# Optimization experiments

Hardware: AMD Instinct MI355X
Metric: run time of the kernel (lower is better)

## Reference

```python
import jax, jax.numpy as jnp
import numpy as np

H = 10                 # heads in both convs
EPS = 1e-5             # GraphNorm eps
N, E, D_NODE, D_EDGE, G = 100000, 1600000, 128, 32, 64


def _lin(key, out_d, in_d, bias=True):
    k1, k2 = jax.random.split(key)
    W = jax.random.normal(k1, (out_d, in_d), jnp.float32) / np.sqrt(in_d)
    if bias:
        b = jax.random.normal(k2, (out_d,), jnp.float32) * 0.01
        return W, b
    return W


def setup_inputs() -> dict:
    key = jax.random.key(0)
    ks = jax.random.split(key, 20)
    x = jax.random.normal(ks[0], (N, D_NODE), jnp.float32)
    edge_attr = jax.random.normal(ks[1], (E, D_EDGE), jnp.float32)
    edge_index = jax.random.randint(ks[2], (2, E), 0, N)
    batch_idx = jnp.sort(jax.random.randint(ks[3], (N,), 0, G))
    # conv1: in=128, out=5, heads=10
    q1W, q1b = _lin(ks[4], H * 5, D_NODE)
    k1W, k1b = _lin(ks[5], H * 5, D_NODE)
    v1W, v1b = _lin(ks[6], H * 5, D_NODE)
    e1W = _lin(ks[7], H * 5, D_EDGE, bias=False)
    s1W, s1b = _lin(ks[8], 5, D_NODE)        # lin_skip
    b1W = _lin(ks[9], 1, 3 * 5, bias=False)  # lin_beta
    # GraphNorm(5)
    gnW = jnp.ones((5,), jnp.float32)
    gnb = jnp.zeros((5,), jnp.float32)
    gnms = jnp.ones((5,), jnp.float32)       # mean_scale
    # conv2: in=5, out=1, heads=10
    q2W, q2b = _lin(ks[10], H * 1, 5)
    k2W, k2b = _lin(ks[11], H * 1, 5)
    v2W, v2b = _lin(ks[12], H * 1, 5)
    e2W = _lin(ks[13], H * 1, D_EDGE, bias=False)
    s2W, s2b = _lin(ks[14], 1, 5)
    b2W = _lin(ks[15], 1, 3 * 1, bias=False)
    return dict(x=x, edge_attr=edge_attr, edge_index=edge_index, batch_idx=batch_idx,
                q1W=q1W, q1b=q1b, k1W=k1W, k1b=k1b, v1W=v1W, v1b=v1b, e1W=e1W,
                s1W=s1W, s1b=s1b, b1W=b1W, gnW=gnW, gnb=gnb, gnms=gnms,
                q2W=q2W, q2b=q2b, k2W=k2W, k2b=k2b, v2W=v2W, v2b=v2b, e2W=e2W,
                s2W=s2W, s2b=s2b, b2W=b2W)


def _tconv(x, src, dst, edge_attr, qW, qb, kW, kb, vW, vb, eW, sW, sb, bW, c):
    """PyG TransformerConv: concat=False, beta=True, eval (dropout off)."""
    n = x.shape[0]
    q = (x @ qW.T + qb).reshape(n, H, c)
    k = (x @ kW.T + kb).reshape(n, H, c)
    v = (x @ vW.T + vb).reshape(n, H, c)
    e = (edge_attr @ eW.T).reshape(-1, H, c)            # [E,H,c]
    kj = k[src] + e                                      # gather + edge bias
    alpha = jnp.einsum('ehc,ehc->eh', q[dst], kj) / np.sqrt(c)
    amax = jax.lax.stop_gradient(jax.ops.segment_max(alpha, dst, num_segments=n))
    ex = jnp.exp(alpha - amax[dst])
    denom = jax.ops.segment_sum(ex, dst, num_segments=n)
    a = ex / denom[dst]                                  # segment softmax [E,H]
    out = jax.ops.segment_sum((v[src] + e) * a[:, :, None], dst, num_segments=n)
    out = out.mean(axis=1)                               # concat=False -> head mean [N,c]
    xr = x @ sW.T + sb                                   # skip
    beta = jax.nn.sigmoid(jnp.concatenate([out, xr, out - xr], -1) @ bW.T)
    return beta * xr + (1.0 - beta) * out


def _graph_norm(x, batch, w, b, ms):
    cnt = jnp.maximum(jax.ops.segment_sum(jnp.ones((x.shape[0],), x.dtype), batch,
                                          num_segments=G), 1.0)[:, None]
    mean = jax.ops.segment_sum(x, batch, num_segments=G) / cnt
    out = x - mean[batch] * ms
    var = jax.ops.segment_sum(out * out, batch, num_segments=G) / cnt
    return w * out / jnp.sqrt(var + EPS)[batch] + b


def reference(x, edge_attr, edge_index, batch_idx,
              q1W, q1b, k1W, k1b, v1W, v1b, e1W, s1W, s1b, b1W,
              gnW, gnb, gnms,
              q2W, q2b, k2W, k2b, v2W, v2b, e2W, s2W, s2b, b2W):
    src, dst = edge_index[0], edge_index[1]
    h = _tconv(x, src, dst, edge_attr, q1W, q1b, k1W, k1b, v1W, v1b, e1W,
               s1W, s1b, b1W, 5)
    h = jax.nn.relu(_graph_norm(h, batch_idx, gnW, gnb, gnms))
    out = _tconv(h, src, dst, edge_attr, q2W, q2b, k2W, k2b, v2W, v2b, e2W,
                 s2W, s2b, b2W, 1)
    return jax.nn.sigmoid(out)
```

## Files before the change

### kernel.cpp

```cpp
#include <hip/hip_runtime.h>
#include <math.h>


#define EPS 1e-5f
#define INV_SQRT5 0.44721359549995794f

__device__ __forceinline__ float f16_to_f32(unsigned short u) {
  union { unsigned short us; _Float16 h; } cv; cv.us = u;
  return (float)cv.h;
}

__device__ __forceinline__ void store40(const float (&acc)[40], int n, int g,
                                        float* __restrict__ q1, float* __restrict__ kv1,
                                        float* __restrict__ xr1) {
#pragma unroll
  for (int c = 0; c < 40; ++c) {
    int ch = g * 40 + c;
    if (ch < 50)        q1[(size_t)n * 52 + ch] = acc[c];
    else if (ch < 100)  kv1[(size_t)n * 104 + 2 * (ch - 50)] = acc[c];
    else if (ch < 150)  kv1[(size_t)n * 104 + 2 * (ch - 100) + 1] = acc[c];
    else if (ch < 155)  xr1[(size_t)n * 8 + (ch - 150)] = acc[c];
  }
}

__global__ __launch_bounds__(256, 4) void k_qkvs1(
    const float* __restrict__ x,
    const float* __restrict__ qW, const float* __restrict__ qb,
    const float* __restrict__ kW, const float* __restrict__ kb,
    const float* __restrict__ vW, const float* __restrict__ vb,
    const float* __restrict__ sW, const float* __restrict__ sb,
    float* __restrict__ q1, float* __restrict__ kv1,
    float* __restrict__ xr1, int n_nodes) {
  __shared__ __align__(16) float sWt[40 * 128];
  __shared__ float sB[40];
  const int t = threadIdx.x;
  const int g = blockIdx.y;
  const int n0 = blockIdx.x * 512;

  for (int i = t; i < 1280; i += 256) {
    int c = i >> 5, q = i & 31;
    int ch = g * 40 + c;
    float4 w = make_float4(0.f, 0.f, 0.f, 0.f);
    const float* srcr = nullptr;
    if (ch < 50)        srcr = qW + ch * 128;
    else if (ch < 100)  srcr = kW + (ch - 50) * 128;
    else if (ch < 150)  srcr = vW + (ch - 100) * 128;
    else if (ch < 155)  srcr = sW + (ch - 150) * 128;
    if (srcr) w = *(const float4*)(srcr + q * 4);
    *(float4*)&sWt[c * 128 + q * 4] = w;
  }
  if (t < 40) {
    int ch = g * 40 + t;
    float b = 0.f;
    if (ch < 50) b = qb[ch];
    else if (ch < 100) b = kb[ch - 50];
    else if (ch < 150) b = vb[ch - 100];
    else if (ch < 155) b = sb[ch - 150];
    sB[t] = b;
  }
  __syncthreads();

  float accA[40], accB[40];
#pragma unroll
  for (int c = 0; c < 40; ++c) { accA[c] = sB[c]; accB[c] = sB[c]; }
  const int na = n0 + 2 * t, nb = na + 1;
  const bool okA = na < n_nodes, okB = nb < n_nodes;
  const float* xa_p = x + (size_t)(okA ? na : 0) * 128;
  const float* xb_p = x + (size_t)(okB ? nb : 0) * 128;
  const float4* w4 = (const float4*)sWt;

  for (int kc = 0; kc < 128; kc += 8) {
    float4 xa0 = *(const float4*)(xa_p + kc);
    float4 xa1 = *(const float4*)(xa_p + kc + 4);
    float4 xb0 = *(const float4*)(xb_p + kc);
    float4 xb1 = *(const float4*)(xb_p + kc + 4);
    const int base = kc >> 2;
#pragma unroll
    for (int c = 0; c < 40; ++c) {
      float4 w0 = w4[c * 32 + base];
      float4 w1 = w4[c * 32 + base + 1];
      accA[c] = fmaf(w0.x, xa0.x, accA[c]); accA[c] = fmaf(w0.y, xa0.y, accA[c]);
      accA[c] = fmaf(w0.z, xa0.z, accA[c]); accA[c] = fmaf(w0.w, xa0.w, accA[c]);
      accA[c] = fmaf(w1.x, xa1.x, accA[c]); accA[c] = fmaf(w1.y, xa1.y, accA[c]);
      accA[c] = fmaf(w1.z, xa1.z, accA[c]); accA[c] = fmaf(w1.w, xa1.w, accA[c]);
      accB[c] = fmaf(w0.x, xb0.x, accB[c]); accB[c] = fmaf(w0.y, xb0.y, accB[c]);
      accB[c] = fmaf(w0.z, xb0.z, accB[c]); accB[c] = fmaf(w0.w, xb0.w, accB[c]);
      accB[c] = fmaf(w1.x, xb1.x, accB[c]); accB[c] = fmaf(w1.y, xb1.y, accB[c]);
      accB[c] = fmaf(w1.w, xb1.w, accB[c]); accB[c] = fmaf(w1.z, xb1.z, accB[c]);
    }
  }
  if (okA) store40(accA, na, g, q1, kv1, xr1);
  if (okB) store40(accB, nb, g, q1, kv1, xr1);
}

__global__ __launch_bounds__(256) void k_hist(const int* __restrict__ ei, int n_edges,
                                              int* __restrict__ cnt) {
  int e = blockIdx.x * 256 + threadIdx.x;
  if (e < n_edges) atomicAdd(&cnt[ei[n_edges + e]], 1);
}

__global__ __launch_bounds__(256) void k_scansum(const int* __restrict__ cnt,
                                                 int* __restrict__ bsum, int n) {
  int base = blockIdx.x * 1024 + threadIdx.x * 4;
  int s = 0;
  if (base + 3 < n) {
    int4 v = *(const int4*)(cnt + base);
    s = v.x + v.y + v.z + v.w;
  } else {
    for (int i = base; i < n && i < base + 4; ++i) s += cnt[i];
  }
#pragma unroll
  for (int off = 32; off; off >>= 1) s += __shfl_down(s, off);
  __shared__ int wsum[4];
  if ((threadIdx.x & 63) == 0) wsum[threadIdx.x >> 6] = s;
  __syncthreads();
  if (threadIdx.x == 0) bsum[blockIdx.x] = wsum[0] + wsum[1] + wsum[2] + wsum[3];
}

__global__ __launch_bounds__(256) void k_scantop(int* __restrict__ bsum, int nb) {
  __shared__ int ls[256];
  int tid = threadIdx.x;
  int v = (tid < nb) ? bsum[tid] : 0;
  ls[tid] = v;
  __syncthreads();
  for (int off = 1; off < 256; off <<= 1) {
    int t = (tid >= off) ? ls[tid - off] : 0;
    __syncthreads();
    ls[tid] += t;
    __syncthreads();
  }
  if (tid < nb) bsum[tid] = ls[tid] - v;
}

__global__ __launch_bounds__(256) void k_scanout(const int* __restrict__ cnt,
                                                 const int* __restrict__ bsum,
                                                 int* __restrict__ rp,
                                                 int* __restrict__ cursor, int n) {
  const int tid = threadIdx.x;
  const int lane = tid & 63;
  const int w = tid >> 6;
  int base = blockIdx.x * 1024 + tid * 4;
  int c0 = 0, c1 = 0, c2 = 0, c3 = 0;
  if (base + 3 < n) {
    int4 v = *(const int4*)(cnt + base);
    c0 = v.x; c1 = v.y; c2 = v.z; c3 = v.w;
  } else if (base < n) {
    c0 = cnt[base];
    if (base + 1 < n) c1 = cnt[base + 1];
    if (base + 2 < n) c2 = cnt[base + 2];
    if (base + 3 < n) c3 = cnt[base + 3];
  }
  int s = c0 + c1 + c2 + c3;
  int incl = s;
#pragma unroll
  for (int off = 1; off < 64; off <<= 1) {
    int t = __shfl_up(incl, off);
    if (lane >= off) incl += t;
  }
  __shared__ int wsum[4];
  if (lane == 63) wsum[w] = incl;
  __syncthreads();
  int woff = 0;
#pragma unroll
  for (int j = 0; j < 3; ++j) if (j < w) woff += wsum[j];
  int excl = bsum[blockIdx.x] + woff + (incl - s);
  int4 o;
  o.x = excl; o.y = o.x + c0; o.z = o.y + c1; o.w = o.z + c2;
  if (base + 3 < n) {
    *(int4*)(rp + base) = o;
    *(int4*)(cursor + base) = o;
  } else if (base < n) {
    rp[base] = o.x; cursor[base] = o.x;
    if (base + 1 < n) { rp[base + 1] = o.y; cursor[base + 1] = o.y; }
    if (base + 2 < n) { rp[base + 2] = o.z; cursor[base + 2] = o.z; }
  }
  if (base < n && base + 4 >= n) rp[n] = excl + s;
}

__global__ __launch_bounds__(256) void k_scatter(const int* __restrict__ ei, int n_edges,
                                                 int* __restrict__ cursor,
                                                 int* __restrict__ seid,
                                                 int* __restrict__ ssrc) {
  int e = blockIdx.x * 256 + threadIdx.x;
  if (e >= n_edges) return;
  int s = ei[e];
  int d = ei[n_edges + e];
  int p = atomicAdd(&cursor[d], 1);
  seid[p] = e;
  ssrc[p] = s;
}

__global__ __launch_bounds__(256) void k_evt(
    float* attr, const float* __restrict__ e1W, const float* __restrict__ e2W,
    int n_edges) {
  int e = blockIdx.x * 256 + threadIdx.x;
  if (e >= n_edges) return;
  const float4* ar = (const float4*)(attr + (size_t)e * 32);
  float4 a[8];
#pragma unroll
  for (int j = 0; j < 8; ++j) a[j] = ar[j];
  unsigned int d[30];
#pragma unroll
  for (int c2 = 0; c2 < 30; ++c2) {
    int c0 = 2 * c2, c1 = 2 * c2 + 1;
    const float* w0 = (c0 < 50) ? (e1W + c0 * 32) : (e2W + (c0 - 50) * 32);
    const float* w1 = (c1 < 50) ? (e1W + c1 * 32) : (e2W + (c1 - 50) * 32);
    float acc0 = 0.f, acc1 = 0.f;
#pragma unroll
    for (int j = 0; j < 8; ++j) {
      float4 wa = *(const float4*)(w0 + 4 * j);
      float4 wb = *(const float4*)(w1 + 4 * j);
      acc0 = fmaf(wa.x, a[j].x, acc0); acc0 = fmaf(wa.y, a[j].y, acc0);
      acc0 = fmaf(wa.z, a[j].z, acc0); acc0 = fmaf(wa.w, a[j].w, acc0);
      acc1 = fmaf(wb.x, a[j].x, acc1); acc1 = fmaf(wb.y, a[j].y, acc1);
      acc1 = fmaf(wb.z, a[j].z, acc1); acc1 = fmaf(wb.w, a[j].w, acc1);
    }
    union { _Float16 h[2]; unsigned int u; } p;
    p.h[0] = (_Float16)acc0; p.h[1] = (_Float16)acc1;
    d[c2] = p.u;
  }
  unsigned int* row = (unsigned int*)(attr + (size_t)e * 32);
#pragma unroll
  for (int k = 0; k < 7; ++k)
    *(uint4*)(row + 4 * k) = make_uint4(d[4 * k], d[4 * k + 1], d[4 * k + 2], d[4 * k + 3]);
  *(uint2*)(row + 28) = make_uint2(d[28], d[29]);
}

__global__ __launch_bounds__(256) void k_conv1(
    const int* __restrict__ rp, const int* __restrict__ seid,
    const int* __restrict__ ssrc, const float* __restrict__ attr,
    const float* __restrict__ q1, const float* __restrict__ kv1,
    const float* __restrict__ xr1,
    const float* __restrict__ bW, float* __restrict__ h1, int n_nodes) {
  const int lane = threadIdx.x & 63;
  const int wid = (blockIdx.x * 256 + threadIdx.x) >> 6;
  const int nw = gridDim.x * 4;
  const int wr = (lane < 50) ? lane : 0;
  const int g0 = (wr / 5) * 5;
  const int cp = lane % 5;
  const unsigned short* evr = (const unsigned short*)attr;

  for (int n = wid; n < n_nodes; n += nw) {
    const int p0 = rp[n], deg = rp[n + 1] - p0;
    const float qc = q1[(size_t)n * 52 + wr];
    int eL = 0, sL = 0;
    if (lane < deg) { eL = seid[p0 + lane]; sL = ssrc[p0 + lane]; }
    float accN0 = 0.f, accD0 = 0.f, accN1 = 0.f, accD1 = 0.f;
    int i = 0;
    for (; i + 2 <= deg; i += 2) {
      int e0, s0, e1, s1;
      if (i + 1 < 64) {
        e0 = __shfl(eL, i);     s0 = __shfl(sL, i);
        e1 = __shfl(eL, i + 1); s1 = __shfl(sL, i + 1);
      } else {
        e0 = (i < 64) ? __shfl(eL, i) : seid[p0 + i];
        s0 = (i < 64) ? __shfl(sL, i) : ssrc[p0 + i];
        e1 = seid[p0 + i + 1];  s1 = ssrc[p0 + i + 1];
      }
      float ev0 = f16_to_f32(evr[(size_t)e0 * 64 + wr]);
      float ev1 = f16_to_f32(evr[(size_t)e1 * 64 + wr]);
      float2 kva = *(const float2*)(kv1 + (size_t)s0 * 104 + 2 * wr);
      float2 kvb = *(const float2*)(kv1 + (size_t)s1 * 104 + 2 * wr);
      float t0 = qc * (kva.x + ev0);
      float t1 = qc * (kvb.x + ev1);
      float al0 = __shfl(t0, g0) + __shfl(t0, g0 + 1) + __shfl(t0, g0 + 2)
                + __shfl(t0, g0 + 3) + __shfl(t0, g0 + 4);
      float al1 = __shfl(t1, g0) + __shfl(t1, g0 + 1) + __shfl(t1, g0 + 2)
                + __shfl(t1, g0 + 3) + __shfl(t1, g0 + 4);
      float ex0 = __expf(al0 * INV_SQRT5);
      float ex1 = __expf(al1 * INV_SQRT5);
      accD0 += ex0; accN0 = fmaf(kva.y + ev0, ex0, accN0);
      accD1 += ex1; accN1 = fmaf(kvb.y + ev1, ex1, accN1);
    }
    if (i < deg) {
      int e = (i < 64) ? __shfl(eL, i) : seid[p0 + i];
      int s = (i < 64) ? __shfl(sL, i) : ssrc[p0 + i];
      float ev = f16_to_f32(evr[(size_t)e * 64 + wr]);
      float2 kv = *(const float2*)(kv1 + (size_t)s * 104 + 2 * wr);
      float t = qc * (kv.x + ev);
      float al = __shfl(t, g0) + __shfl(t, g0 + 1) + __shfl(t, g0 + 2)
               + __shfl(t, g0 + 3) + __shfl(t, g0 + 4);
      float ex = __expf(al * INV_SQRT5);
      accD0 += ex; accN0 = fmaf(kv.y + ev, ex, accN0);
    }
    float accN = accN0 + accN1, accD = accD0 + accD1;
    float r = (accD > 0.f) ? accN / accD : 0.f;
    if (lane >= 50) r = 0.f;
    float o = 0.f;
#pragma unroll
    for (int h = 0; h < 10; ++h) o += __shfl(r, cp + 5 * h);
    o *= 0.1f;
    float xr = xr1[(size_t)n * 8 + cp];
    float tb = bW[cp] * o + bW[5 + cp] * xr + bW[10 + cp] * (o - xr);
    float sb = 0.f;
#pragma unroll
    for (int j = 0; j < 5; ++j) sb += __shfl(tb, j);
    float beta = 1.f / (1.f + __expf(-sb));
    if (lane < 5) h1[(size_t)n * 8 + lane] = beta * xr + (1.f - beta) * o;
  }
}

__global__ __launch_bounds__(256) void k_stats(
    const float* __restrict__ h1, const int* __restrict__ batch,
    float* __restrict__ gsum, float* __restrict__ gsq,
    float* __restrict__ gcnt, int n_nodes) {
  int n = blockIdx.x * 256 + threadIdx.x;
  bool act = n < n_nodes;
  int g = act ? batch[n] : 0;
  float v[5], s2[5], one = act ? 1.f : 0.f;
#pragma unroll
  for (int c = 0; c < 5; ++c) {
    v[c] = act ? h1[(size_t)n * 8 + c] : 0.f;
    s2[c] = v[c] * v[c];
  }
  int g0 = __shfl(g, 0);
  bool uni = __all((!act) || (g == g0));
  if (uni) {
#pragma unroll
    for (int off = 32; off; off >>= 1) {
#pragma unroll
      for (int c = 0; c < 5; ++c) {
        v[c] += __shfl_down(v[c], off);
        s2[c] += __shfl_down(s2[c], off);
      }
      one += __shfl_down(one, off);
    }
    if ((threadIdx.x & 63) == 0) {
#pragma unroll
      for (int c = 0; c < 5; ++c) {
        atomicAdd(&gsum[g0 * 8 + c], v[c]);
        atomicAdd(&gsq[g0 * 8 + c], s2[c]);
      }
      atomicAdd(&gcnt[g0], one);
    }
  } else if (act) {
#pragma unroll
    for (int c = 0; c < 5; ++c) {
      atomicAdd(&gsum[g * 8 + c], v[c]);
      atomicAdd(&gsq[g * 8 + c], s2[c]);
    }
    atomicAdd(&gcnt[g], 1.f);
  }
}

__global__ __launch_bounds__(256) void k_apply(
    const float* __restrict__ h1, const int* __restrict__ batch,
    const float* __restrict__ gsum, const float* __restrict__ gsq,
    const float* __restrict__ gcnt,
    const float* __restrict__ gnw, const float* __restrict__ gnb,
    const float* __restrict__ gnms,
    const float* __restrict__ q2W, const float* __restrict__ q2b,
    const float* __restrict__ k2W, const float* __restrict__ k2b,
    const float* __restrict__ v2W, const float* __restrict__ v2b,
    const float* __restrict__ s2W, const float* __restrict__ s2b,
    float* __restrict__ q2, float* __restrict__ kv2,
    float* __restrict__ xr2, int n_nodes) {
  int n = blockIdx.x * 256 + threadIdx.x;
  if (n >= n_nodes) return;
  int g = batch[n];
  float rc = 1.f / fmaxf(gcnt[g], 1.f);
  float r[5];
#pragma unroll
  for (int c = 0; c < 5; ++c) {
    float ms = gnms[c];
    float mean = gsum[g * 8 + c] * rc;
    float var = gsq[g * 8 + c] * rc - mean * mean * ms * (2.f - ms);
    var = fmaxf(var, 0.f);
    float o = h1[(size_t)n * 8 + c] - mean * ms;
    float y = gnw[c] * o * rsqrtf(var + EPS) + gnb[c];
    r[c] = fmaxf(y, 0.f);
  }
#pragma unroll
  for (int h = 0; h < 10; ++h) {
    float aq = q2b[h], ak = k2b[h], av = v2b[h];
#pragma unroll
    for (int i = 0; i < 5; ++i) {
      aq = fmaf(r[i], q2W[h * 5 + i], aq);
      ak = fmaf(r[i], k2W[h * 5 + i], ak);
      av = fmaf(r[i], v2W[h * 5 + i], av);
    }
    q2[(size_t)n * 12 + h] = aq;
    kv2[(size_t)n * 24 + 2 * h]     = ak;
    kv2[(size_t)n * 24 + 2 * h + 1] = av;
  }
  float s = s2b[0];
#pragma unroll
  for (int i = 0; i < 5; ++i) s = fmaf(r[i], s2W[i], s);
  xr2[n] = s;
}

__global__ __launch_bounds__(256) void k_conv2(
    const int* __restrict__ rp, const int* __restrict__ seid,
    const int* __restrict__ ssrc, const float* __restrict__ attr,
    const float* __restrict__ q2, const float* __restrict__ kv2,
    const float* __restrict__ xr2,
    const float* __restrict__ bW, float* __restrict__ out, int n_nodes) {
  const int lane = threadIdx.x & 63;
  const int wid = (blockIdx.x * 256 + threadIdx.x) >> 6;
  const int nw = gridDim.x * 4;
  const int slot = lane / 10, h = lane - slot * 10;
  const bool active = slot < 6;
  const unsigned short* evr = (const unsigned short*)attr;

  for (int n = wid; n < n_nodes; n += nw) {
    int p0 = rp[n], deg = rp[n + 1] - p0;
    float qh = q2[(size_t)n * 12 + h];
    int eL = 0, sL = 0;
    if (lane < deg) { eL = seid[p0 + lane]; sL = ssrc[p0 + lane]; }
    float accN = 0.f, accD = 0.f;
    int nit = (deg + 5) / 6;
    for (int t = 0; t < nit; ++t) {
      int i = t * 6 + slot;
      bool val = active && (i < deg);
      int e = 0, s = 0;
      if (i < 64) { e = __shfl(eL, i); s = __shfl(sL, i); }
      else if (val) { e = seid[p0 + i]; s = ssrc[p0 + i]; }
      float evv = 0.f; float2 kv = make_float2(0.f, 0.f);
      if (val) {
        evv = f16_to_f32(evr[(size_t)e * 64 + 50 + h]);
        kv = *(const float2*)(kv2 + (size_t)s * 24 + 2 * h);
      }
      float exv = val ? __expf(qh * (kv.x + evv)) : 0.f;
      accD += exv;
      accN = fmaf(kv.y + evv, exv, accN);
    }
    float D = 0.f, Nn = 0.f;
#pragma unroll
    for (int i2 = 0; i2 < 6; ++i2) {
      D  += __shfl(accD, h + 10 * i2);
      Nn += __shfl(accN, h + 10 * i2);
    }
    float r = (D > 0.f) ? Nn / D : 0.f;
    float o = 0.f;
#pragma unroll
    for (int j = 0; j < 10; ++j) o += __shfl(r, j);
    o *= 0.1f;
    float xr = xr2[n];
    float sbv = bW[0] * o + bW[1] * xr + bW[2] * (o - xr);
    float beta = 1.f / (1.f + __expf(-sbv));
    float y = beta * xr + (1.f - beta) * o;
    if (lane == 0) out[n] = 1.f / (1.f + __expf(-y));
  }
}

extern "C" void kernel_launch(void* const* d_in, const int* in_sizes, int n_in,
                              void* d_out, int out_size, void* d_ws, size_t ws_size,
                              hipStream_t stream) {
  const float* x    = (const float*)d_in[0];
  float*       attr = (float*)d_in[1];
  const int*   ei   = (const int*)d_in[2];
  const int*   batch= (const int*)d_in[3];
  const float* q1W = (const float*)d_in[4];  const float* q1b = (const float*)d_in[5];
  const float* k1W = (const float*)d_in[6];  const float* k1b = (const float*)d_in[7];
  const float* v1W = (const float*)d_in[8];  const float* v1b = (const float*)d_in[9];
  const float* e1W = (const float*)d_in[10];
  const float* s1W = (const float*)d_in[11]; const float* s1b = (const float*)d_in[12];
  const float* b1W = (const float*)d_in[13];
  const float* gnW = (const float*)d_in[14]; const float* gnb = (const float*)d_in[15];
  const float* gnms= (const float*)d_in[16];
  const float* q2W = (const float*)d_in[17]; const float* q2b = (const float*)d_in[18];
  const float* k2W = (const float*)d_in[19]; const float* k2b = (const float*)d_in[20];
  const float* v2W = (const float*)d_in[21]; const float* v2b = (const float*)d_in[22];
  const float* e2W = (const float*)d_in[23];
  const float* s2W = (const float*)d_in[24]; const float* s2b = (const float*)d_in[25];
  const float* b2W = (const float*)d_in[26];

  const int n_nodes = in_sizes[0] / 128;
  const int n_edges = in_sizes[2] / 2;
  float* ws = (float*)d_ws;
  const size_t nn = (size_t)n_nodes;
  const size_t ne = (size_t)n_edges;

  const size_t oQ1  = 0;
  const size_t oKV1 = 52 * nn;
  const size_t oXR1 = 156 * nn;
  const size_t oH1  = 164 * nn;
  const size_t oQ2  = 172 * nn;
  const size_t oKV2 = 184 * nn;
  const size_t oXR2 = 208 * nn;
  const size_t oSTAT= 209 * nn;
  const size_t oCNT = oSTAT + 1088;
  const size_t oRP  = oCNT + nn;
  const size_t oCUR = oRP + nn + 4;
  const size_t oSEID= oCUR + nn;
  const size_t oSSRC= oSEID + ne;
  const size_t oBSUM= oSSRC + ne;

  int* cnt    = (int*)(ws + oCNT);
  int* rp     = (int*)(ws + oRP);
  int* cursor = (int*)(ws + oCUR);
  int* seid   = (int*)(ws + oSEID);
  int* ssrc   = (int*)(ws + oSSRC);
  int* bsum   = (int*)(ws + oBSUM);
  float* gsum = ws + oSTAT;
  float* gsq  = ws + oSTAT + 512;
  float* gcnt = ws + oSTAT + 1024;

  const int nb_nodes = (n_nodes + 255) / 256;
  const int nb_edges = (n_edges + 255) / 256;
  const int nb_scan  = (n_nodes + 1023) / 1024;
  dim3 gq((n_nodes + 511) / 512, 4);
  const int nb_pers = 2048;

  hipMemsetAsync(ws + oSTAT, 0, (1088 + nn) * sizeof(float), stream);

  k_hist<<<nb_edges, 256, 0, stream>>>(ei, n_edges, cnt);
  k_scansum<<<nb_scan, 256, 0, stream>>>(cnt, bsum, n_nodes);
  k_scantop<<<1, 256, 0, stream>>>(bsum, nb_scan);
  k_scanout<<<nb_scan, 256, 0, stream>>>(cnt, bsum, rp, cursor, n_nodes);
  k_scatter<<<nb_edges, 256, 0, stream>>>(ei, n_edges, cursor, seid, ssrc);

  k_qkvs1<<<gq, 256, 0, stream>>>(x, q1W, q1b, k1W, k1b, v1W, v1b, s1W, s1b,
                                  ws + oQ1, ws + oKV1, ws + oXR1, n_nodes);
  k_evt<<<nb_edges, 256, 0, stream>>>(attr, e1W, e2W, n_edges);

  k_conv1<<<nb_pers, 256, 0, stream>>>(rp, seid, ssrc, attr,
                                       ws + oQ1, ws + oKV1, ws + oXR1,
                                       b1W, ws + oH1, n_nodes);
  k_stats<<<nb_nodes, 256, 0, stream>>>(ws + oH1, batch, gsum, gsq, gcnt, n_nodes);
  k_apply<<<nb_nodes, 256, 0, stream>>>(ws + oH1, batch, gsum, gsq, gcnt,
                                        gnW, gnb, gnms,
                                        q2W, q2b, k2W, k2b, v2W, v2b, s2W, s2b,
                                        ws + oQ2, ws + oKV2, ws + oXR2, n_nodes);
  k_conv2<<<nb_pers, 256, 0, stream>>>(rp, seid, ssrc, attr,
                                       ws + oQ2, ws + oKV2, ws + oXR2,
                                       b2W, (float*)d_out, n_nodes);
}
```

Before: 1.064 ms.

## Remap conv1 aggregation lanes to edge-slot by head with per-lane 5-dim dot

Rewrites the conv1 attention aggregation so each wavefront processes 6 edges at once, with 10 lanes per edge each owning one head's 5 channels. Each lane computes its head's dot product locally instead of using 5 cross-lane shuffles per edge, and prefetches the next edge index. Partial sums from the 6 edge slots are combined with shuffles at the end. The cost is more per-lane gather work (strided fp16 and float2 loads), 4 of 64 lanes left idle, and a shuffle reduction per node. A reordering of two FMAs in the projection kernel is also included and is only cosmetic.

```diff
diff --git a/kernel.cpp b/kernel.cpp
--- a/kernel.cpp
+++ b/kernel.cpp
@@ -86,7 +86,7 @@
       accB[c] = fmaf(w0.x, xb0.x, accB[c]); accB[c] = fmaf(w0.y, xb0.y, accB[c]);
       accB[c] = fmaf(w0.z, xb0.z, accB[c]); accB[c] = fmaf(w0.w, xb0.w, accB[c]);
       accB[c] = fmaf(w1.x, xb1.x, accB[c]); accB[c] = fmaf(w1.y, xb1.y, accB[c]);
-      accB[c] = fmaf(w1.w, xb1.w, accB[c]); accB[c] = fmaf(w1.z, xb1.z, accB[c]);
+      accB[c] = fmaf(w1.z, xb1.z, accB[c]); accB[c] = fmaf(w1.w, xb1.w, accB[c]);
     }
   }
   if (okA) store40(accA, na, g, q1, kv1, xr1);
@@ -235,68 +235,103 @@
   const int lane = threadIdx.x & 63;
   const int wid = (blockIdx.x * 256 + threadIdx.x) >> 6;
   const int nw = gridDim.x * 4;
-  const int wr = (lane < 50) ? lane : 0;
-  const int g0 = (wr / 5) * 5;
-  const int cp = lane % 5;
-  const unsigned short* evr = (const unsigned short*)attr;
+  const int slot = lane / 10;
+  const int h = lane - slot * 10;
+  const bool active = slot < 6;
+  const int cs = 5 * h;
+  const unsigned int* evu = (const unsigned int*)attr;
+
+  float bw0[5], bw1[5], bw2[5];
+#pragma unroll
+  for (int c = 0; c < 5; ++c) { bw0[c] = bW[c]; bw1[c] = bW[5 + c]; bw2[c] = bW[10 + c]; }
 
   for (int n = wid; n < n_nodes; n += nw) {
     const int p0 = rp[n], deg = rp[n + 1] - p0;
-    const float qc = q1[(size_t)n * 52 + wr];
-    int eL = 0, sL = 0;
-    if (lane < deg) { eL = seid[p0 + lane]; sL = ssrc[p0 + lane]; }
-    float accN0 = 0.f, accD0 = 0.f, accN1 = 0.f, accD1 = 0.f;
-    int i = 0;
-    for (; i + 2 <= deg; i += 2) {
-      int e0, s0, e1, s1;
-      if (i + 1 < 64) {
-        e0 = __shfl(eL, i);     s0 = __shfl(sL, i);
-        e1 = __shfl(eL, i + 1); s1 = __shfl(sL, i + 1);
-      } else {
-        e0 = (i < 64) ? __shfl(eL, i) : seid[p0 + i];
-        s0 = (i < 64) ? __shfl(sL, i) : ssrc[p0 + i];
-        e1 = seid[p0 + i + 1];  s1 = ssrc[p0 + i + 1];
+    const float* qp = q1 + (size_t)n * 52 + cs;
+    const float q0 = qp[0], q1v = qp[1], q2v = qp[2], q3v = qp[3], q4v = qp[4];
+
+    float accD = 0.f, aN0 = 0.f, aN1 = 0.f, aN2 = 0.f, aN3 = 0.f, aN4 = 0.f;
+    const int nit = (deg + 5) / 6;
+    int i = slot;
+    bool val = active && (i < deg);
+    int e = 0, s = 0;
+    if (val) { e = seid[p0 + i]; s = ssrc[p0 + i]; }
+    for (int t = 0; t < nit; ++t) {
+      int in = i + 6;
+      bool valn = active && (in < deg);
+      int en = 0, sn = 0;
+      if (valn) { en = seid[p0 + in]; sn = ssrc[p0 + in]; }
+      float ev0 = 0.f, ev1 = 0.f, ev2 = 0.f, ev3 = 0.f, ev4 = 0.f;
+      float2 kv0 = make_float2(0.f, 0.f), kv1v = kv0, kv2v = kv0, kv3v = kv0, kv4v = kv0;
+      if (val) {
+        const unsigned int* er = evu + (size_t)e * 32 + (cs >> 1);
+        unsigned int u0 = er[0], u1 = er[1], u2 = er[2];
+        if (cs & 1) {
+          ev0 = f16_to_f32((unsigned short)(u0 >> 16));
+          ev1 = f16_to_f32((unsigned short)(u1 & 0xffff));
+          ev2 = f16_to_f32((unsigned short)(u1 >> 16));
+          ev3 = f16_to_f32((unsigned short)(u2 & 0xffff));
+          ev4 = f16_to_f32((unsigned short)(u2 >> 16));
+        } else {
+          ev0 = f16_to_f32((unsigned short)(u0 & 0xffff));
+          ev1 = f16_to_f32((unsigned short)(u0 >> 16));
+          ev2 = f16_to_f32((unsigned short)(u1 & 0xffff));
+          ev3 = f16_to_f32((unsigned short)(u1 >> 16));
+          ev4 = f16_to_f32((unsigned short)(u2 & 0xffff));
+        }
+        const float* kvp = kv1 + (size_t)s * 104 + 10 * h;
+        kv0 = *(const float2*)(kvp);
+        kv1v = *(const float2*)(kvp + 2);
+        kv2v = *(const float2*)(kvp + 4);
+        kv3v = *(const float2*)(kvp + 6);
+        kv4v = *(const float2*)(kvp + 8);
       }
-      float ev0 = f16_to_f32(evr[(size_t)e0 * 64 + wr]);
-      float ev1 = f16_to_f32(evr[(size_t)e1 * 64 + wr]);
-      float2 kva = *(const float2*)(kv1 + (size_t)s0 * 104 + 2 * wr);
-      float2 kvb = *(const float2*)(kv1 + (size_t)s1 * 104 + 2 * wr);
-      float t0 = qc * (kva.x + ev0);
-      float t1 = qc * (kvb.x + ev1);
-      float al0 = __shfl(t0, g0) + __shfl(t0, g0 + 1) + __shfl(t0, g0 + 2)
-                + __shfl(t0, g0 + 3) + __shfl(t0, g0 + 4);
-      float al1 = __shfl(t1, g0) + __shfl(t1, g0 + 1) + __shfl(t1, g0 + 2)
-                + __shfl(t1, g0 + 3) + __shfl(t1, g0 + 4);
-      float ex0 = __expf(al0 * INV_SQRT5);
-      float ex1 = __expf(al1 * INV_SQRT5);
-      accD0 += ex0; accN0 = fmaf(kva.y + ev0, ex0, accN0);
-      accD1 += ex1; accN1 = fmaf(kvb.y + ev1, ex1, accN1);
-    }
-    if (i < deg) {
-      int e = (i < 64) ? __shfl(eL, i) : seid[p0 + i];
-      int s = (i < 64) ? __shfl(sL, i) : ssrc[p0 + i];
-      float ev = f16_to_f32(evr[(size_t)e * 64 + wr]);
-      float2 kv = *(const float2*)(kv1 + (size_t)s * 104 + 2 * wr);
-      float t = qc * (kv.x + ev);
-      float al = __shfl(t, g0) + __shfl(t, g0 + 1) + __shfl(t, g0 + 2)
-               + __shfl(t, g0 + 3) + __shfl(t, g0 + 4);
-      float ex = __expf(al * INV_SQRT5);
-      accD0 += ex; accN0 = fmaf(kv.y + ev, ex, accN0);
-    }
-    float accN = accN0 + accN1, accD = accD0 + accD1;
-    float r = (accD > 0.f) ? accN / accD : 0.f;
-    if (lane >= 50) r = 0.f;
-    float o = 0.f;
-#pragma unroll
-    for (int h = 0; h < 10; ++h) o += __shfl(r, cp + 5 * h);
-    o *= 0.1f;
-    float xr = xr1[(size_t)n * 8 + cp];
-    float tb = bW[cp] * o + bW[5 + cp] * xr + bW[10 + cp] * (o - xr);
-    float sb = 0.f;
-#pragma unroll
-    for (int j = 0; j < 5; ++j) sb += __shfl(tb, j);
+      float al = q0 * (kv0.x + ev0);
+      al = fmaf(q1v, kv1v.x + ev1, al);
+      al = fmaf(q2v, kv2v.x + ev2, al);
+      al = fmaf(q3v, kv3v.x + ev3, al);
+      al = fmaf(q4v, kv4v.x + ev4, al);
+      float ex = val ? __expf(al * INV_SQRT5) : 0.f;
+      accD += ex;
+      aN0 = fmaf(kv0.y + ev0, ex, aN0);
+      aN1 = fmaf(kv1v.y + ev1, ex, aN1);
+      aN2 = fmaf(kv2v.y + ev2, ex, aN2);
+      aN3 = fmaf(kv3v.y + ev3, ex, aN3);
+      aN4 = fmaf(kv4v.y + ev4, ex, aN4);
+      i = in; val = valn; e = en; s = sn;
+    }
+    float D = 0.f, N0 = 0.f, N1 = 0.f, N2 = 0.f, N3 = 0.f, N4 = 0.f;
+#pragma unroll
+    for (int i2 = 0; i2 < 6; ++i2) {
+      int sl = h + 10 * i2;
+      D  += __shfl(accD, sl);
+      N0 += __shfl(aN0, sl); N1 += __shfl(aN1, sl); N2 += __shfl(aN2, sl);
+      N3 += __shfl(aN3, sl); N4 += __shfl(aN4, sl);
+    }
+    float rD = (D > 0.f) ? (1.f / D) : 0.f;
+    float r0 = N0 * rD, r1 = N1 * rD, r2 = N2 * rD, r3 = N3 * rD, r4 = N4 * rD;
+    float o0 = 0.f, o1 = 0.f, o2 = 0.f, o3 = 0.f, o4 = 0.f;
+#pragma unroll
+    for (int hh = 0; hh < 10; ++hh) {
+      o0 += __shfl(r0, hh); o1 += __shfl(r1, hh); o2 += __shfl(r2, hh);
+      o3 += __shfl(r3, hh); o4 += __shfl(r4, hh);
+    }
+    o0 *= 0.1f; o1 *= 0.1f; o2 *= 0.1f; o3 *= 0.1f; o4 *= 0.1f;
+    float4 xv = *(const float4*)(xr1 + (size_t)n * 8);
+    float x4 = xr1[(size_t)n * 8 + 4];
+    float sb = bw0[0] * o0 + bw1[0] * xv.x + bw2[0] * (o0 - xv.x);
+    sb += bw0[1] * o1 + bw1[1] * xv.y + bw2[1] * (o1 - xv.y);
+    sb += bw0[2] * o2 + bw1[2] * xv.z + bw2[2] * (o2 - xv.z);
+    sb += bw0[3] * o3 + bw1[3] * xv.w + bw2[3] * (o3 - xv.w);
+    sb += bw0[4] * o4 + bw1[4] * x4 + bw2[4] * (o4 - x4);
     float beta = 1.f / (1.f + __expf(-sb));
-    if (lane < 5) h1[(size_t)n * 8 + lane] = beta * xr + (1.f - beta) * o;
+    if (lane < 5) {
+      float ow = (lane == 0) ? o0 : (lane == 1) ? o1 : (lane == 2) ? o2
+               : (lane == 3) ? o3 : o4;
+      float xw = (lane == 0) ? xv.x : (lane == 1) ? xv.y : (lane == 2) ? xv.z
+               : (lane == 3) ? xv.w : x4;
+      h1[(size_t)n * 8 + lane] = beta * xw + (1.f - beta) * ow;
+    }
   }
 }
 
```

Result: no change. 1.062 ms (-0.2%).
